# Kernel optimization log

Hardware: AMD Instinct MI355X
Metric: run time of the kernel (lower is better)

## Reference

```python
import jax, jax.numpy as jnp
import numpy as np

TOPK = 2
NUM_BODY_POINTS = 17
HIDDEN = 64


def bilinear_grid_sample(feat, grid):
    """F.grid_sample(feat, grid, mode='bilinear', padding_mode='zeros', align_corners=False).
    feat: [B,C,H,W]; grid: [B,L,K,2] in [-1,1], grid[...,0]=x (width), grid[...,1]=y (height).
    Returns [B,C,L,K]."""
    B, C, H, W = feat.shape
    x = (grid[..., 0] + 1.0) * (0.5 * W) - 0.5  # [B,L,K]
    y = (grid[..., 1] + 1.0) * (0.5 * H) - 0.5
    x0 = jnp.floor(x)
    y0 = jnp.floor(y)
    wx1 = x - x0
    wy1 = y - y0
    featf = feat.reshape(B, C, H * W)

    def gather(xi, yi):
        valid = (xi >= 0) & (xi < W) & (yi >= 0) & (yi < H)  # [B,L,K]
        xc = jnp.clip(xi, 0, W - 1).astype(jnp.int32)
        yc = jnp.clip(yi, 0, H - 1).astype(jnp.int32)
        idx = (yc * W + xc).reshape(B, -1)  # [B, L*K]
        v = jax.vmap(lambda f, i: f[:, i])(featf, idx)  # [B,C,L*K]
        v = v.reshape(B, C, *xi.shape[1:])  # [B,C,L,K]
        return v * valid[:, None].astype(feat.dtype)

    w00 = ((1 - wx1) * (1 - wy1))[:, None]
    w10 = (wx1 * (1 - wy1))[:, None]
    w01 = ((1 - wx1) * wy1)[:, None]
    w11 = (wx1 * wy1)[:, None]
    return (gather(x0, y0) * w00 + gather(x0 + 1, y0) * w10
            + gather(x0, y0 + 1) * w01 + gather(x0 + 1, y0 + 1) * w11)


def setup_inputs() -> dict:
    key = jax.random.key(0)
    ks = jax.random.split(key, 8)
    B, L, K, C, H, Wd = 16, 1000, NUM_BODY_POINTS, 17, 256, 256
    in_dim = K * (TOPK + 1)
    scores = jax.random.normal(ks[0], (B, L, 1), dtype=jnp.float32)
    pred_poses = jax.random.uniform(ks[1], (B, L, 2 * K), dtype=jnp.float32)
    feat = jax.random.normal(ks[2], (B, C, H, Wd), dtype=jnp.float32)
    s1 = 1.0 / np.sqrt(in_dim)
    s2 = 1.0 / np.sqrt(HIDDEN)
    w1 = jax.random.uniform(ks[3], (HIDDEN, in_dim), minval=-s1, maxval=s1, dtype=jnp.float32)
    b1 = jax.random.uniform(ks[4], (HIDDEN,), minval=-s1, maxval=s1, dtype=jnp.float32)
    w2 = jax.random.uniform(ks[5], (1, HIDDEN), minval=-s2, maxval=s2, dtype=jnp.float32)
    b2 = jax.random.uniform(ks[6], (1,), minval=-s2, maxval=s2, dtype=jnp.float32)
    return {"scores": scores, "pred_poses": pred_poses, "feat": feat,
            "w1": w1, "b1": b1, "w2": w2, "b2": b2}


def reference(scores, pred_poses, feat, w1, b1, w2, b2):
    B, L = pred_poses.shape[:2]
    poses = pred_poses.reshape(B, L, NUM_BODY_POINTS, 2)
    sampled = bilinear_grid_sample(feat, 2.0 * poses - 1.0)  # [B,C,L,K]
    sampled = jnp.transpose(sampled, (0, 2, 3, 1))  # [B,L,K,C]
    prob_topk, _ = jax.lax.top_k(sampled, TOPK)  # [B,L,K,topk]
    stat = jnp.concatenate([prob_topk, prob_topk.mean(axis=-1, keepdims=True)], axis=-1)
    x = stat.reshape(B, L, -1)  # [B,L,K*(topk+1)]
    h = jax.nn.relu(jnp.einsum('bli,hi->blh', x, w1) + b1)
    quality = jnp.einsum('blh,oh->blo', h, w2) + b2  # [B,L,1]
    return scores + quality
```

## Files before the change

kernel.cpp:

```cpp
#include <hip/hip_runtime.h>
#include <hip/hip_bf16.h>
#include <math.h>

#define NB 16
#define NL 1000
#define NK 17
#define NC 17
#define NH 256
#define NW 256
#define HID 64
#define IN_DIM 51
#define PPB 15
#define NPAIR (NB*NL)
#define PADC 20

__global__ __launch_bounds__(256) void transpose_feat(
    const float* __restrict__ feat, float* __restrict__ featT)
{
    __shared__ float s[NC][257];
    const int b    = blockIdx.x >> 8;
    const int hw0  = (blockIdx.x & 255) * 256;
    const int tid  = threadIdx.x;
    const float* fb = feat + (size_t)b * NC * (NH * NW) + hw0;
    #pragma unroll
    for (int c = 0; c < NC; ++c)
        s[c][tid] = fb[c * (NH * NW) + tid];
    __syncthreads();
    float4* outp = reinterpret_cast<float4*>(
        featT + ((size_t)b * (NH * NW) + hw0) * PADC);
    #pragma unroll
    for (int i = tid; i < 256 * PADC / 4; i += 256) {
        const int p = i / 5;
        const int j = i - 5 * p;
        float4 v;
        if (j < 4) {
            const int c = 4 * j;
            v = make_float4(s[c][p], s[c + 1][p], s[c + 2][p], s[c + 3][p]);
        } else {
            v = make_float4(s[16][p], 0.f, 0.f, 0.f);
        }
        outp[i] = v;
    }
}

__global__ __launch_bounds__(256) void lqe_fused_t(
    const float* __restrict__ scores,
    const float* __restrict__ pred_poses,
    const float* __restrict__ featT,
    const float* __restrict__ w1,
    const float* __restrict__ b1,
    const float* __restrict__ w2,
    const float* __restrict__ b2,
    float* __restrict__ out)
{
    __shared__ float s_w1[HID * IN_DIM];
    __shared__ float s_b1[HID];
    __shared__ float s_w2[HID];
    __shared__ float s_x[PPB][IN_DIM + 1];

    const int tid = threadIdx.x;
    for (int i = tid; i < HID * IN_DIM; i += 256) s_w1[i] = w1[i];
    if (tid < HID) { s_b1[tid] = b1[tid]; s_w2[tid] = w2[tid]; }

    if (tid < PPB * NK) {
        const int lp = tid / NK;
        const int k  = tid - lp * NK;
        const int pair = blockIdx.x * PPB + lp;
        if (pair < NPAIR) {
            const int b = pair / NL;
            const float2 p = *reinterpret_cast<const float2*>(
                pred_poses + (size_t)pair * (2 * NK) + 2 * k);
            const float gx = 2.0f * p.x - 1.0f;
            const float gy = 2.0f * p.y - 1.0f;
            const float fx = (gx + 1.0f) * (0.5f * NW) - 0.5f;
            const float fy = (gy + 1.0f) * (0.5f * NH) - 0.5f;
            const float x0f = floorf(fx), y0f = floorf(fy);
            const float wx = fx - x0f,   wy = fy - y0f;
            const int ix0 = (int)x0f, iy0 = (int)y0f;
            const int ix1 = ix0 + 1,  iy1 = iy0 + 1;
            const float vx0 = (ix0 >= 0 && ix0 < NW) ? 1.f : 0.f;
            const float vx1 = (ix1 >= 0 && ix1 < NW) ? 1.f : 0.f;
            const float vy0 = (iy0 >= 0 && iy0 < NH) ? 1.f : 0.f;
            const float vy1 = (iy1 >= 0 && iy1 < NH) ? 1.f : 0.f;
            const float w00 = (1.f - wx) * (1.f - wy) * vx0 * vy0;
            const float w10 = wx * (1.f - wy) * vx1 * vy0;
            const float w01 = (1.f - wx) * wy * vx0 * vy1;
            const float w11 = wx * wy * vx1 * vy1;
            const int cx0 = min(max(ix0, 0), NW - 1), cx1 = min(max(ix1, 0), NW - 1);
            const int cy0 = min(max(iy0, 0), NH - 1), cy1 = min(max(iy1, 0), NH - 1);
            const float* fb = featT + (size_t)b * (NH * NW) * PADC;
            const float* p00 = fb + (size_t)(cy0 * NW + cx0) * PADC;
            const float* p10 = fb + (size_t)(cy0 * NW + cx1) * PADC;
            const float* p01 = fb + (size_t)(cy1 * NW + cx0) * PADC;
            const float* p11 = fb + (size_t)(cy1 * NW + cx1) * PADC;

            float v00[NC], v10[NC], v01[NC], v11[NC];
            #pragma unroll
            for (int j = 0; j < 4; ++j) {
                *reinterpret_cast<float4*>(&v00[4 * j]) =
                    *reinterpret_cast<const float4*>(p00 + 4 * j);
                *reinterpret_cast<float4*>(&v10[4 * j]) =
                    *reinterpret_cast<const float4*>(p10 + 4 * j);
                *reinterpret_cast<float4*>(&v01[4 * j]) =
                    *reinterpret_cast<const float4*>(p01 + 4 * j);
                *reinterpret_cast<float4*>(&v11[4 * j]) =
                    *reinterpret_cast<const float4*>(p11 + 4 * j);
            }
            v00[16] = p00[16]; v10[16] = p10[16];
            v01[16] = p01[16]; v11[16] = p11[16];

            float m1 = -INFINITY, m2 = -INFINITY;
            #pragma unroll
            for (int c = 0; c < NC; ++c) {
                const float v = w00 * v00[c] + w10 * v10[c]
                              + w01 * v01[c] + w11 * v11[c];
                if (v > m1)      { m2 = m1; m1 = v; }
                else if (v > m2) { m2 = v; }
            }
            s_x[lp][3 * k + 0] = m1;
            s_x[lp][3 * k + 1] = m2;
            s_x[lp][3 * k + 2] = 0.5f * (m1 + m2);
        }
    }
    __syncthreads();

    const int wv = tid >> 6;
    const int lane = tid & 63;
    const float vb2 = b2[0];
    for (int lp = wv; lp < PPB; lp += 4) {
        const int pair = blockIdx.x * PPB + lp;
        if (pair >= NPAIR) break;
        float h = s_b1[lane];
        #pragma unroll
        for (int i = 0; i < IN_DIM; ++i)
            h = fmaf(s_x[lp][i], s_w1[lane * IN_DIM + i], h);
        h = fmaxf(h, 0.f);
        float pval = h * s_w2[lane];
        #pragma unroll
        for (int off = 32; off >= 1; off >>= 1)
            pval += __shfl_xor(pval, off, 64);
        if (lane == 0) out[pair] = scores[pair] + pval + vb2;
    }
}

__global__ __launch_bounds__(256) void lqe_fused_direct(
    const float* __restrict__ scores,
    const float* __restrict__ pred_poses,
    const float* __restrict__ feat,
    const float* __restrict__ w1,
    const float* __restrict__ b1,
    const float* __restrict__ w2,
    const float* __restrict__ b2,
    float* __restrict__ out)
{
    __shared__ float s_w1[HID * IN_DIM];
    __shared__ float s_b1[HID];
    __shared__ float s_w2[HID];
    __shared__ float s_x[PPB][IN_DIM + 1];

    const int tid = threadIdx.x;
    for (int i = tid; i < HID * IN_DIM; i += 256) s_w1[i] = w1[i];
    if (tid < HID) { s_b1[tid] = b1[tid]; s_w2[tid] = w2[tid]; }

    if (tid < PPB * NK) {
        const int lp = tid / NK;
        const int k  = tid - lp * NK;
        const int pair = blockIdx.x * PPB + lp;
        if (pair < NPAIR) {
            const int b = pair / NL;
            const float2 p = *reinterpret_cast<const float2*>(
                pred_poses + (size_t)pair * (2 * NK) + 2 * k);
            const float gx = 2.0f * p.x - 1.0f;
            const float gy = 2.0f * p.y - 1.0f;
            const float fx = (gx + 1.0f) * (0.5f * NW) - 0.5f;
            const float fy = (gy + 1.0f) * (0.5f * NH) - 0.5f;
            const float x0f = floorf(fx), y0f = floorf(fy);
            const float wx = fx - x0f,   wy = fy - y0f;
            const int ix0 = (int)x0f, iy0 = (int)y0f;
            const int ix1 = ix0 + 1,  iy1 = iy0 + 1;
            const float vx0 = (ix0 >= 0 && ix0 < NW) ? 1.f : 0.f;
            const float vx1 = (ix1 >= 0 && ix1 < NW) ? 1.f : 0.f;
            const float vy0 = (iy0 >= 0 && iy0 < NH) ? 1.f : 0.f;
            const float vy1 = (iy1 >= 0 && iy1 < NH) ? 1.f : 0.f;
            const float w00 = (1.f - wx) * (1.f - wy) * vx0 * vy0;
            const float w10 = wx * (1.f - wy) * vx1 * vy0;
            const float w01 = (1.f - wx) * wy * vx0 * vy1;
            const float w11 = wx * wy * vx1 * vy1;
            const int cx0 = min(max(ix0, 0), NW - 1), cx1 = min(max(ix1, 0), NW - 1);
            const int cy0 = min(max(iy0, 0), NH - 1), cy1 = min(max(iy1, 0), NH - 1);
            const int o00 = cy0 * NW + cx0, o10 = cy0 * NW + cx1;
            const int o01 = cy1 * NW + cx0, o11 = cy1 * NW + cx1;
            const float* fb = feat + (size_t)b * NC * NH * NW;
            float m1 = -INFINITY, m2 = -INFINITY;
            #pragma unroll
            for (int c = 0; c < NC; ++c) {
                const float* fc = fb + c * (NH * NW);
                const float v = w00 * fc[o00] + w10 * fc[o10]
                              + w01 * fc[o01] + w11 * fc[o11];
                if (v > m1)      { m2 = m1; m1 = v; }
                else if (v > m2) { m2 = v; }
            }
            s_x[lp][3 * k + 0] = m1;
            s_x[lp][3 * k + 1] = m2;
            s_x[lp][3 * k + 2] = 0.5f * (m1 + m2);
        }
    }
    __syncthreads();

    const int wv = tid >> 6;
    const int lane = tid & 63;
    const float vb2 = b2[0];
    for (int lp = wv; lp < PPB; lp += 4) {
        const int pair = blockIdx.x * PPB + lp;
        if (pair >= NPAIR) break;
        float h = s_b1[lane];
        #pragma unroll
        for (int i = 0; i < IN_DIM; ++i)
            h = fmaf(s_x[lp][i], s_w1[lane * IN_DIM + i], h);
        h = fmaxf(h, 0.f);
        float pval = h * s_w2[lane];
        #pragma unroll
        for (int off = 32; off >= 1; off >>= 1)
            pval += __shfl_xor(pval, off, 64);
        if (lane == 0) out[pair] = scores[pair] + pval + vb2;
    }
}

extern "C" void kernel_launch(void* const* d_in, const int* in_sizes, int n_in,
                              void* d_out, int out_size, void* d_ws, size_t ws_size,
                              hipStream_t stream) {
    const float* scores     = (const float*)d_in[0];
    const float* pred_poses = (const float*)d_in[1];
    const float* feat       = (const float*)d_in[2];
    const float* w1         = (const float*)d_in[3];
    const float* b1         = (const float*)d_in[4];
    const float* w2         = (const float*)d_in[5];
    const float* b2         = (const float*)d_in[6];
    float* out = (float*)d_out;

    const int grid = (NPAIR + PPB - 1) / PPB;
    const size_t needT = (size_t)NB * NH * NW * PADC * sizeof(float);

    if (ws_size >= needT) {
        float* featT = (float*)d_ws;
        transpose_feat<<<NB * 256, 256, 0, stream>>>(feat, featT);
        lqe_fused_t<<<grid, 256, 0, stream>>>(scores, pred_poses, featT,
                                              w1, b1, w2, b2, out);
    } else {
        lqe_fused_direct<<<grid, 256, 0, stream>>>(scores, pred_poses, feat,
                                                   w1, b1, w2, b2, out);
    }
}
```

Measured before the change: 157.6 us.

## Remap blocks so each XCD handles a contiguous batch slice for L2 locality

Both the transpose and fused kernels now remap blockIdx so that blocks landing on the same XCD (round-robin by blockIdx mod 8) work on a contiguous range of batches. Each XCD then writes and reads the transposed feature map for only two batch images, which keeps those gathers in that XCD's private L2 instead of spreading across all eight. It also streams the bilinear top-2 directly from the float4 loads instead of staging 68 values in register arrays, which should lower register pressure. The mapping depends on the hardware's round-robin block dispatch assumption and the fixed problem sizes.

```diff
diff --git a/kernel.cpp b/kernel.cpp
--- a/kernel.cpp
+++ b/kernel.cpp
@@ -13,14 +13,21 @@
 #define PPB 15
 #define NPAIR (NB*NL)
 #define PADC 20
+#define PAIRS_PER_XCD 2000
+#define BLKS_PER_XCD 134
+
+#define TOP2(v) do { const float _v = (v); \
+    if (_v > m1) { m2 = m1; m1 = _v; } else if (_v > m2) { m2 = _v; } } while (0)
 
 __global__ __launch_bounds__(256) void transpose_feat(
     const float* __restrict__ feat, float* __restrict__ featT)
 {
     __shared__ float s[NC][257];
-    const int b    = blockIdx.x >> 8;
-    const int hw0  = (blockIdx.x & 255) * 256;
-    const int tid  = threadIdx.x;
+    const int bid = blockIdx.x;
+    const int l   = ((bid & 7) << 9) | (bid >> 3);
+    const int b   = l >> 8;
+    const int hw0 = (l & 255) << 8;
+    const int tid = threadIdx.x;
     const float* fb = feat + (size_t)b * NC * (NH * NW) + hw0;
     #pragma unroll
     for (int c = 0; c < NC; ++c)
@@ -59,14 +66,19 @@
     __shared__ float s_x[PPB][IN_DIM + 1];
 
     const int tid = threadIdx.x;
+    const int xcd    = blockIdx.x & 7;
+    const int idx    = blockIdx.x >> 3;
+    const int local0 = idx * PPB;
+
     for (int i = tid; i < HID * IN_DIM; i += 256) s_w1[i] = w1[i];
     if (tid < HID) { s_b1[tid] = b1[tid]; s_w2[tid] = w2[tid]; }
 
     if (tid < PPB * NK) {
         const int lp = tid / NK;
         const int k  = tid - lp * NK;
-        const int pair = blockIdx.x * PPB + lp;
-        if (pair < NPAIR) {
+        const int local = local0 + lp;
+        if (local < PAIRS_PER_XCD) {
+            const int pair = xcd * PAIRS_PER_XCD + local;
             const int b = pair / NL;
             const float2 p = *reinterpret_cast<const float2*>(
                 pred_poses + (size_t)pair * (2 * NK) + 2 * k);
@@ -94,29 +106,20 @@
             const float* p01 = fb + (size_t)(cy1 * NW + cx0) * PADC;
             const float* p11 = fb + (size_t)(cy1 * NW + cx1) * PADC;
 
-            float v00[NC], v10[NC], v01[NC], v11[NC];
+            float m1 = -INFINITY, m2 = -INFINITY;
             #pragma unroll
             for (int j = 0; j < 4; ++j) {
-                *reinterpret_cast<float4*>(&v00[4 * j]) =
-                    *reinterpret_cast<const float4*>(p00 + 4 * j);
-                *reinterpret_cast<float4*>(&v10[4 * j]) =
-                    *reinterpret_cast<const float4*>(p10 + 4 * j);
-                *reinterpret_cast<float4*>(&v01[4 * j]) =
-                    *reinterpret_cast<const float4*>(p01 + 4 * j);
-                *reinterpret_cast<float4*>(&v11[4 * j]) =
-                    *reinterpret_cast<const float4*>(p11 + 4 * j);
+                const float4 a = *reinterpret_cast<const float4*>(p00 + 4 * j);
+                const float4 bq = *reinterpret_cast<const float4*>(p10 + 4 * j);
+                const float4 c = *reinterpret_cast<const float4*>(p01 + 4 * j);
+                const float4 d = *reinterpret_cast<const float4*>(p11 + 4 * j);
+                TOP2(w00 * a.x + w10 * bq.x + w01 * c.x + w11 * d.x);
+                TOP2(w00 * a.y + w10 * bq.y + w01 * c.y + w11 * d.y);
+                TOP2(w00 * a.z + w10 * bq.z + w01 * c.z + w11 * d.z);
+                TOP2(w00 * a.w + w10 * bq.w + w01 * c.w + w11 * d.w);
             }
-            v00[16] = p00[16]; v10[16] = p10[16];
-            v01[16] = p01[16]; v11[16] = p11[16];
-
-            float m1 = -INFINITY, m2 = -INFINITY;
-            #pragma unroll
-            for (int c = 0; c < NC; ++c) {
-                const float v = w00 * v00[c] + w10 * v10[c]
-                              + w01 * v01[c] + w11 * v11[c];
-                if (v > m1)      { m2 = m1; m1 = v; }
-                else if (v > m2) { m2 = v; }
-            }
+            TOP2(w00 * p00[16] + w10 * p10[16] + w01 * p01[16] + w11 * p11[16]);
+
             s_x[lp][3 * k + 0] = m1;
             s_x[lp][3 * k + 1] = m2;
             s_x[lp][3 * k + 2] = 0.5f * (m1 + m2);
@@ -128,8 +131,8 @@
     const int lane = tid & 63;
     const float vb2 = b2[0];
     for (int lp = wv; lp < PPB; lp += 4) {
-        const int pair = blockIdx.x * PPB + lp;
-        if (pair >= NPAIR) break;
+        if (local0 + lp >= PAIRS_PER_XCD) break;
+        const int pair = xcd * PAIRS_PER_XCD + local0 + lp;
         float h = s_b1[lane];
         #pragma unroll
         for (int i = 0; i < IN_DIM; ++i)
@@ -195,10 +198,7 @@
             #pragma unroll
             for (int c = 0; c < NC; ++c) {
                 const float* fc = fb + c * (NH * NW);
-                const float v = w00 * fc[o00] + w10 * fc[o10]
-                              + w01 * fc[o01] + w11 * fc[o11];
-                if (v > m1)      { m2 = m1; m1 = v; }
-                else if (v > m2) { m2 = v; }
+                TOP2(w00 * fc[o00] + w10 * fc[o10] + w01 * fc[o01] + w11 * fc[o11]);
             }
             s_x[lp][3 * k + 0] = m1;
             s_x[lp][3 * k + 1] = m2;
@@ -238,15 +238,15 @@
     const float* b2         = (const float*)d_in[6];
     float* out = (float*)d_out;
 
-    const int grid = (NPAIR + PPB - 1) / PPB;
     const size_t needT = (size_t)NB * NH * NW * PADC * sizeof(float);
 
     if (ws_size >= needT) {
         float* featT = (float*)d_ws;
         transpose_feat<<<NB * 256, 256, 0, stream>>>(feat, featT);
-        lqe_fused_t<<<grid, 256, 0, stream>>>(scores, pred_poses, featT,
-                                              w1, b1, w2, b2, out);
+        lqe_fused_t<<<8 * BLKS_PER_XCD, 256, 0, stream>>>(
+            scores, pred_poses, featT, w1, b1, w2, b2, out);
     } else {
+        const int grid = (NPAIR + PPB - 1) / PPB;
         lqe_fused_direct<<<grid, 256, 0, stream>>>(scores, pred_poses, feat,
                                                    w1, b1, w2, b2, out);
     }
```

After: 163.6 us. 1.04x slower.
